# Performance work log

Hardware: AMD Instinct MI355X
Metric: run time of the kernel (lower is better)

The kernel has to match this reference:

```python
import jax, jax.numpy as jnp
import numpy as np

GRID_SIZE = 5
SPLINE_ORDER = 3
GRID_RANGE = (-1.0, 1.0)


def b_splines(x, grid, spline_order=SPLINE_ORDER):
    # x: [B, in], grid: [G] with G = grid_size + 2*spline_order + 1
    x = x[..., None]                      # [B, in, 1]
    g = grid[None, None, :]               # [1, 1, G]
    bases = ((x >= g[..., :-1]) & (x < g[..., 1:])).astype(x.dtype)  # [B, in, G-1]
    for k in range(1, spline_order + 1):
        left = (x - g[..., :-(k + 1)]) / (g[..., k:-1] - g[..., :-(k + 1)]) * bases[..., :-1]
        right = (g[..., k + 1:] - x) / (g[..., k + 1:] - g[..., 1:-k]) * bases[..., 1:]
        bases = left + right
    return bases                          # [B, in, grid_size + spline_order]


def setup_inputs() -> dict:
    key = jax.random.key(0)
    k1, k2, k3, k4 = jax.random.split(key, 4)
    B, IN, OUT = 32768, 256, 256
    n_coef = GRID_SIZE + SPLINE_ORDER  # 8
    h = (GRID_RANGE[1] - GRID_RANGE[0]) / GRID_SIZE
    grid = jnp.arange(-SPLINE_ORDER, GRID_SIZE + SPLINE_ORDER + 1, dtype=jnp.float32) * h + GRID_RANGE[0]  # [12]
    x = jax.random.normal(k1, (B, IN), dtype=jnp.float32)
    base_weight = jax.random.normal(k2, (OUT, IN), dtype=jnp.float32) * np.sqrt(2.0 / IN)
    spline_weight = jax.random.normal(k3, (OUT, IN, n_coef), dtype=jnp.float32) * (0.1 / GRID_SIZE)
    spline_scaler = jax.random.normal(k4, (OUT, IN), dtype=jnp.float32) * np.sqrt(2.0 / IN)
    return {"x": x, "base_weight": base_weight, "spline_weight": spline_weight,
            "spline_scaler": spline_scaler, "grid": grid}


def reference(x, base_weight, spline_weight, spline_scaler, grid):
    B = x.shape[0]
    out_features = base_weight.shape[0]
    # base branch: silu(x) @ base_weight^T
    base_out = jnp.matmul(jax.nn.silu(x), base_weight.T)  # [B, out]
    # spline branch
    bases = b_splines(x, grid)                             # [B, in, n_coef]
    scaled_w = spline_weight * spline_scaler[..., None]    # [out, in, n_coef]
    spline_out = jnp.matmul(bases.reshape(B, -1), scaled_w.reshape(out_features, -1).T)
    return base_out + spline_out
```

## Files before the change

### kernel.cpp

```cpp
#include <hip/hip_runtime.h>
#include <stdint.h>


#define IN_F 256
#define OUT_F 256
#define KDIM 2304
#define BK 64
#define NCHUNK (KDIM / BK)

typedef float f32x4 __attribute__((ext_vector_type(4)));
typedef short bf16x8 __attribute__((ext_vector_type(8)));

__device__ __forceinline__ uint32_t f2bf(float f) {
    union { float f; uint32_t u; } c; c.f = f;
    uint32_t u = c.u;
    return (u + 0x7FFFu + ((u >> 16) & 1u)) >> 16;
}

__device__ __forceinline__ uint32_t cvtpk(float lo, float hi) {
    uint32_t r;
    asm("v_cvt_pk_bf16_f32 %0, %1, %2" : "=v"(r) : "v"(lo), "v"(hi));
    return r;
}

__device__ __forceinline__ float silu_f(float v) {
    return v / (1.0f + __expf(-v));
}

__device__ __forceinline__ void block_sync_lds() {
    __builtin_amdgcn_sched_barrier(0);
    asm volatile("s_waitcnt lgkmcnt(0)" ::: "memory");
    __builtin_amdgcn_sched_barrier(0);
    __builtin_amdgcn_s_barrier();
    __builtin_amdgcn_sched_barrier(0);
}

__device__ __forceinline__ uint4 basis16(float xx) {
    float u = __builtin_fmaf(xx, 2.5f, 5.5f);
    float jf = floorf(u);
    float t = u - jf;
    int j0 = (int)jf;
    float t2 = t * t, t3 = t2 * t;
    float p3 = t3 * (1.0f / 6.0f);
    float p2 = __builtin_fmaf(t3, -0.5f,
               __builtin_fmaf(t2, 0.5f, __builtin_fmaf(t, 0.5f, 1.0f / 6.0f)));
    float p1 = __builtin_fmaf(t3, 0.5f, __builtin_fmaf(t2, -1.0f, 2.0f / 3.0f));
    float omt = 1.0f - t;
    float p0 = omt * omt * omt * (1.0f / 6.0f);
    const int s0 = j0 - 3;
    int ds = s0 >> 1;
    if ((unsigned)j0 > 10u) ds = 9;
    const bool odd = (s0 & 1) != 0;
    uint32_t v0 = cvtpk(odd ? 0.0f : p0, odd ? p0 : p1);
    uint32_t v1 = cvtpk(odd ? p1 : p2, odd ? p2 : p3);
    uint32_t v2 = odd ? cvtpk(p3, 0.0f) : 0u;
    uint4 r;
    r.x = (ds == 0) ? v0 : (ds == -1) ? v1 : (ds == -2) ? v2 : 0u;
    r.y = (ds == 1) ? v0 : (ds ==  0) ? v1 : (ds == -1) ? v2 : 0u;
    r.z = (ds == 2) ? v0 : (ds ==  1) ? v1 : (ds ==  0) ? v2 : 0u;
    r.w = (ds == 3) ? v0 : (ds ==  2) ? v1 : (ds ==  1) ? v2 : 0u;
    return r;
}

__device__ __forceinline__ size_t wcf_addr(int col, int k) {
    const int kc = k >> 6, kkh = (k >> 5) & 1, q = (k >> 3) & 3, e = k & 7;
    return ((size_t)((kc * 2 + kkh) * 16 + (col >> 4))) * 512 +
           (size_t)(q * 16 + (col & 15)) * 8 + e;
}

__global__ void build_w(const float* __restrict__ bw, const float* __restrict__ sw,
                        const float* __restrict__ ss, unsigned short* __restrict__ WcF) {
    const int o = blockIdx.x;
    const int i = threadIdx.x;
    WcF[wcf_addr(o, i)] = (unsigned short)f2bf(bw[o * IN_F + i]);
    const float scal = ss[o * IN_F + i];
    const float4* swv = reinterpret_cast<const float4*>(sw + (size_t)(o * IN_F + i) * 8);
    float4 s0 = swv[0], s1 = swv[1];
    uint4 wv;
    wv.x = f2bf(s0.x * scal) | (f2bf(s0.y * scal) << 16);
    wv.y = f2bf(s0.z * scal) | (f2bf(s0.w * scal) << 16);
    wv.z = f2bf(s1.x * scal) | (f2bf(s1.y * scal) << 16);
    wv.w = f2bf(s1.z * scal) | (f2bf(s1.w * scal) << 16);
    *reinterpret_cast<uint4*>(WcF + wcf_addr(o, IN_F + i * 8)) = wv;
}

__launch_bounds__(512, 2)
__global__ void kan_fused(const float* __restrict__ x, const unsigned short* __restrict__ WcF,
                          float* __restrict__ out) {
    __shared__ __align__(16) unsigned short As[4][128 * 64];

    const int bid = blockIdx.x;
    const int row0 = bid * 128;
    const int tid = threadIdx.x;
    const int lane = tid & 63;
    const int w = tid >> 6;
    const int wm = w >> 2;
    const int wn = w & 3;
    const int l15 = lane & 15;
    const int q = lane >> 4;

    const int erow = tid >> 2;
    const int qd   = tid & 3;

    f32x4 acc[4][4] = {};
    bf16x8 bE[8], bO[8];
    float2 x0, x1, x2, x3;

    const unsigned short* wbase = WcF + (size_t)lane * 8;

    auto load_b = [&](int kc, bf16x8* dst) {
#pragma unroll
        for (int nt = 0; nt < 4; ++nt)
#pragma unroll
            for (int kkh = 0; kkh < 2; ++kkh)
                dst[nt * 2 + kkh] = *reinterpret_cast<const bf16x8*>(
                    wbase + ((size_t)((kc * 2 + kkh) * 16 + wn * 4 + nt)) * 512);
    };
    auto load_x_silu = [&](int c, float4* xs4) {
        const float* xp = x + (size_t)(row0 + erow) * IN_F + c * 64 + qd * 16;
#pragma unroll
        for (int i = 0; i < 4; ++i)
            xs4[i] = reinterpret_cast<const float4*>(xp)[i];
    };
    auto load_x_bas = [&](int c, float2& v) {
        v = *reinterpret_cast<const float2*>(
            x + (size_t)(row0 + erow) * IN_F + (c - 4) * 8 + qd * 2);
    };
    auto expand_silu = [&](const float4* xs4, uint4& w0, uint4& w1) {
        w0.x = cvtpk(silu_f(xs4[0].x), silu_f(xs4[0].y));
        w0.y = cvtpk(silu_f(xs4[0].z), silu_f(xs4[0].w));
        w0.z = cvtpk(silu_f(xs4[1].x), silu_f(xs4[1].y));
        w0.w = cvtpk(silu_f(xs4[1].z), silu_f(xs4[1].w));
        w1.x = cvtpk(silu_f(xs4[2].x), silu_f(xs4[2].y));
        w1.y = cvtpk(silu_f(xs4[2].z), silu_f(xs4[2].w));
        w1.z = cvtpk(silu_f(xs4[3].x), silu_f(xs4[3].y));
        w1.w = cvtpk(silu_f(xs4[3].z), silu_f(xs4[3].w));
    };
    auto expand_bas = [&](float2 v, uint4& w0, uint4& w1) {
        w0 = basis16(v.x);
        w1 = basis16(v.y);
    };
    auto write_a = [&](unsigned short* Ab, const uint4& w0, const uint4& w1) {
        const int g0 = qd * 2;
        *reinterpret_cast<uint4*>(Ab + erow * 64 + ((g0 ^ (erow & 7)) << 3)) = w0;
        *reinterpret_cast<uint4*>(Ab + erow * 64 + (((g0 + 1) ^ (erow & 7)) << 3)) = w1;
    };
    auto mfma_chunk = [&](const unsigned short* Ab, const bf16x8* bv) {
#pragma unroll
        for (int kkh = 0; kkh < 2; ++kkh) {
            const int g0 = kkh * 4 + q;
#pragma unroll
            for (int mt = 0; mt < 4; ++mt) {
                int r = wm * 64 + mt * 16 + l15;
                bf16x8 a = *reinterpret_cast<const bf16x8*>(
                    Ab + r * 64 + ((g0 ^ (r & 7)) << 3));
                __builtin_amdgcn_s_setprio(1);
#pragma unroll
                for (int nt = 0; nt < 4; ++nt)
                    acc[mt][nt] = __builtin_amdgcn_mfma_f32_16x16x32_bf16(
                        a, bv[nt * 2 + kkh], acc[mt][nt], 0, 0, 0);
                __builtin_amdgcn_s_setprio(0);
            }
        }
    };

    float4 xf2[4], xf3[4];
    {
        float4 t4[4]; uint4 a, b;
        load_x_silu(0, t4); expand_silu(t4, a, b); write_a(&As[0][0], a, b);
        load_x_silu(1, t4); expand_silu(t4, a, b); write_a(&As[1][0], a, b);
    }
    load_x_silu(2, xf2);
    load_x_silu(3, xf3);
    load_x_bas(4, x0);
    load_x_bas(5, x1);
    load_b(0, bE);
    block_sync_lds();

    load_b(1, bO);
    load_x_bas(6, x2);
    load_x_bas(7, x3);
    {
        uint4 a2, b2, a3, b3;
        expand_silu(xf2, a2, b2); expand_silu(xf3, a3, b3);
        write_a(&As[2][0], a2, b2); write_a(&As[3][0], a3, b3);
    }
    mfma_chunk(&As[0][0], bE);
    load_b(2, bE);
    mfma_chunk(&As[1][0], bO);
    block_sync_lds();

    for (int t = 0; t < 8; ++t) {
        {
            const int kc = 4 * t + 2;
            load_b(kc + 1, bO);
            load_x_bas(kc + 4, x2);
            load_x_bas(kc + 5, x3);
            uint4 wa0, wb0, wa1, wb1;
            if (w < 4) {
                expand_bas(x0, wa0, wb0); expand_bas(x1, wa1, wb1);
                write_a(&As[0][0], wa0, wb0); write_a(&As[1][0], wa1, wb1);
                mfma_chunk(&As[2][0], bE);
                load_b(kc + 2, bE);
                mfma_chunk(&As[3][0], bO);
            } else {
                mfma_chunk(&As[2][0], bE);
                load_b(kc + 2, bE);
                mfma_chunk(&As[3][0], bO);
                expand_bas(x0, wa0, wb0); expand_bas(x1, wa1, wb1);
                write_a(&As[0][0], wa0, wb0); write_a(&As[1][0], wa1, wb1);
            }
            block_sync_lds();
        }
        {
            const int kc2 = 4 * t + 4;
            load_b(kc2 + 1, bO);
            if (kc2 + 5 < NCHUNK) {
                load_x_bas(kc2 + 4, x0);
                load_x_bas(kc2 + 5, x1);
            }
            uint4 wa0, wb0, wa1, wb1;
            if (w < 4) {
                expand_bas(x2, wa0, wb0); expand_bas(x3, wa1, wb1);
                write_a(&As[2][0], wa0, wb0); write_a(&As[3][0], wa1, wb1);
                mfma_chunk(&As[0][0], bE);
                load_b(kc2 + 2, bE);
                mfma_chunk(&As[1][0], bO);
            } else {
                mfma_chunk(&As[0][0], bE);
                load_b(kc2 + 2, bE);
                mfma_chunk(&As[1][0], bO);
                expand_bas(x2, wa0, wb0); expand_bas(x3, wa1, wb1);
                write_a(&As[2][0], wa0, wb0); write_a(&As[3][0], wa1, wb1);
            }
            block_sync_lds();
        }
    }

    load_b(35, bO);
    mfma_chunk(&As[2][0], bE);
    mfma_chunk(&As[3][0], bO);

#pragma unroll
    for (int mt = 0; mt < 4; ++mt) {
        int row = row0 + wm * 64 + mt * 16 + q * 4;
#pragma unroll
        for (int nt = 0; nt < 4; ++nt) {
            int col = wn * 64 + nt * 16 + l15;
#pragma unroll
            for (int r = 0; r < 4; ++r)
                out[(size_t)(row + r) * OUT_F + col] = acc[mt][nt][r];
        }
    }
}

extern "C" void kernel_launch(void* const* d_in, const int* in_sizes, int n_in,
                              void* d_out, int out_size, void* d_ws, size_t ws_size,
                              hipStream_t stream) {
    const float* x  = (const float*)d_in[0];
    const float* bw = (const float*)d_in[1];
    const float* sw = (const float*)d_in[2];
    const float* ss = (const float*)d_in[3];
    unsigned short* WcF = (unsigned short*)d_ws;

    build_w<<<dim3(OUT_F), dim3(IN_F), 0, stream>>>(bw, sw, ss, WcF);

    const int B_ROWS = in_sizes[0] / IN_F;
    kan_fused<<<dim3(B_ROWS / 128), dim3(512), 0, stream>>>(
        x, WcF, (float*)d_out);
}
```

Before: 137.1 us.

## Split K across wave groups with 64-row tiles and LDS reduction

Each block now covers 64 rows instead of 128. The two groups of four waves each handle one half of every 64-wide K chunk, and their partial accumulators are summed through LDS at the end. LDS use is halved and occupancy is targeted at 4 blocks per CU, aiming for more latency hiding and more blocks in flight. The cost is twice the B-weight traffic per output row, plus extra barriers and LDS round-trips for the reduction.

```diff
diff --git a/kernel.cpp b/kernel.cpp
--- a/kernel.cpp
+++ b/kernel.cpp
@@ -84,106 +84,91 @@
     *reinterpret_cast<uint4*>(WcF + wcf_addr(o, IN_F + i * 8)) = wv;
 }
 
-__launch_bounds__(512, 2)
+__launch_bounds__(512, 4)
 __global__ void kan_fused(const float* __restrict__ x, const unsigned short* __restrict__ WcF,
                           float* __restrict__ out) {
-    __shared__ __align__(16) unsigned short As[4][128 * 64];
+    __shared__ __align__(16) unsigned short As[4][64 * 64];
 
     const int bid = blockIdx.x;
-    const int row0 = bid * 128;
+    const int row0 = bid * 64;
     const int tid = threadIdx.x;
     const int lane = tid & 63;
     const int w = tid >> 6;
-    const int wm = w >> 2;
+    const int kh = w >> 2;
     const int wn = w & 3;
     const int l15 = lane & 15;
     const int q = lane >> 4;
 
-    const int erow = tid >> 2;
-    const int qd   = tid & 3;
+    const int erow = tid >> 3;
+    const int g8   = tid & 7;
 
     f32x4 acc[4][4] = {};
-    bf16x8 bE[8], bO[8];
-    float2 x0, x1, x2, x3;
+    bf16x8 bE[4], bO[4];
+    float x0, x1, x2, x3;
 
     const unsigned short* wbase = WcF + (size_t)lane * 8;
 
     auto load_b = [&](int kc, bf16x8* dst) {
 #pragma unroll
         for (int nt = 0; nt < 4; ++nt)
-#pragma unroll
-            for (int kkh = 0; kkh < 2; ++kkh)
-                dst[nt * 2 + kkh] = *reinterpret_cast<const bf16x8*>(
-                    wbase + ((size_t)((kc * 2 + kkh) * 16 + wn * 4 + nt)) * 512);
-    };
-    auto load_x_silu = [&](int c, float4* xs4) {
-        const float* xp = x + (size_t)(row0 + erow) * IN_F + c * 64 + qd * 16;
-#pragma unroll
-        for (int i = 0; i < 4; ++i)
-            xs4[i] = reinterpret_cast<const float4*>(xp)[i];
-    };
-    auto load_x_bas = [&](int c, float2& v) {
-        v = *reinterpret_cast<const float2*>(
-            x + (size_t)(row0 + erow) * IN_F + (c - 4) * 8 + qd * 2);
-    };
-    auto expand_silu = [&](const float4* xs4, uint4& w0, uint4& w1) {
-        w0.x = cvtpk(silu_f(xs4[0].x), silu_f(xs4[0].y));
-        w0.y = cvtpk(silu_f(xs4[0].z), silu_f(xs4[0].w));
-        w0.z = cvtpk(silu_f(xs4[1].x), silu_f(xs4[1].y));
-        w0.w = cvtpk(silu_f(xs4[1].z), silu_f(xs4[1].w));
-        w1.x = cvtpk(silu_f(xs4[2].x), silu_f(xs4[2].y));
-        w1.y = cvtpk(silu_f(xs4[2].z), silu_f(xs4[2].w));
-        w1.z = cvtpk(silu_f(xs4[3].x), silu_f(xs4[3].y));
-        w1.w = cvtpk(silu_f(xs4[3].z), silu_f(xs4[3].w));
-    };
-    auto expand_bas = [&](float2 v, uint4& w0, uint4& w1) {
-        w0 = basis16(v.x);
-        w1 = basis16(v.y);
-    };
-    auto write_a = [&](unsigned short* Ab, const uint4& w0, const uint4& w1) {
-        const int g0 = qd * 2;
-        *reinterpret_cast<uint4*>(Ab + erow * 64 + ((g0 ^ (erow & 7)) << 3)) = w0;
-        *reinterpret_cast<uint4*>(Ab + erow * 64 + (((g0 + 1) ^ (erow & 7)) << 3)) = w1;
+            dst[nt] = *reinterpret_cast<const bf16x8*>(
+                wbase + ((size_t)((kc * 2 + kh) * 16 + wn * 4 + nt)) * 512);
+    };
+    auto load_x_silu = [&](int c, float4& a, float4& b) {
+        const float* xp = x + (size_t)(row0 + erow) * IN_F + c * 64 + g8 * 8;
+        a = reinterpret_cast<const float4*>(xp)[0];
+        b = reinterpret_cast<const float4*>(xp)[1];
+    };
+    auto load_x_bas = [&](int c, float& v) {
+        v = x[(size_t)(row0 + erow) * IN_F + (c - 4) * 8 + g8];
+    };
+    auto expand_silu = [&](float4 a, float4 b, uint4& w0) {
+        w0.x = cvtpk(silu_f(a.x), silu_f(a.y));
+        w0.y = cvtpk(silu_f(a.z), silu_f(a.w));
+        w0.z = cvtpk(silu_f(b.x), silu_f(b.y));
+        w0.w = cvtpk(silu_f(b.z), silu_f(b.w));
+    };
+    auto write_a = [&](unsigned short* Ab, const uint4& w0) {
+        *reinterpret_cast<uint4*>(Ab + erow * 64 + ((g8 ^ (erow & 7)) << 3)) = w0;
     };
     auto mfma_chunk = [&](const unsigned short* Ab, const bf16x8* bv) {
-#pragma unroll
-        for (int kkh = 0; kkh < 2; ++kkh) {
-            const int g0 = kkh * 4 + q;
-#pragma unroll
-            for (int mt = 0; mt < 4; ++mt) {
-                int r = wm * 64 + mt * 16 + l15;
-                bf16x8 a = *reinterpret_cast<const bf16x8*>(
-                    Ab + r * 64 + ((g0 ^ (r & 7)) << 3));
-                __builtin_amdgcn_s_setprio(1);
-#pragma unroll
-                for (int nt = 0; nt < 4; ++nt)
-                    acc[mt][nt] = __builtin_amdgcn_mfma_f32_16x16x32_bf16(
-                        a, bv[nt * 2 + kkh], acc[mt][nt], 0, 0, 0);
-                __builtin_amdgcn_s_setprio(0);
-            }
-        }
-    };
-
-    float4 xf2[4], xf3[4];
+        const int g0 = kh * 4 + q;
+#pragma unroll
+        for (int mt = 0; mt < 4; ++mt) {
+            int r = mt * 16 + l15;
+            bf16x8 a = *reinterpret_cast<const bf16x8*>(
+                Ab + r * 64 + ((g0 ^ (r & 7)) << 3));
+            __builtin_amdgcn_s_setprio(1);
+#pragma unroll
+            for (int nt = 0; nt < 4; ++nt)
+                acc[mt][nt] = __builtin_amdgcn_mfma_f32_16x16x32_bf16(
+                    a, bv[nt], acc[mt][nt], 0, 0, 0);
+            __builtin_amdgcn_s_setprio(0);
+        }
+    };
+
+    float4 s2a, s2b, s3a, s3b;
     {
-        float4 t4[4]; uint4 a, b;
-        load_x_silu(0, t4); expand_silu(t4, a, b); write_a(&As[0][0], a, b);
-        load_x_silu(1, t4); expand_silu(t4, a, b); write_a(&As[1][0], a, b);
-    }
-    load_x_silu(2, xf2);
-    load_x_silu(3, xf3);
-    load_x_bas(4, x0);
-    load_x_bas(5, x1);
-    load_b(0, bE);
+        float4 a, b; uint4 t;
+        load_x_silu(0, a, b);
+        load_x_silu(1, s2a, s2b);
+        load_x_silu(2, s3a, s3b);
+        load_b(0, bE);
+        load_x_bas(4, x0);
+        load_x_bas(5, x1);
+        expand_silu(a, b, t);          write_a(&As[0][0], t);
+        expand_silu(s2a, s2b, t);      write_a(&As[1][0], t);
+        load_x_silu(3, s2a, s2b);
+    }
     block_sync_lds();
 
     load_b(1, bO);
-    load_x_bas(6, x2);
-    load_x_bas(7, x3);
     {
-        uint4 a2, b2, a3, b3;
-        expand_silu(xf2, a2, b2); expand_silu(xf3, a3, b3);
-        write_a(&As[2][0], a2, b2); write_a(&As[3][0], a3, b3);
+        uint4 a2, a3;
+        expand_silu(s3a, s3b, a2);
+        expand_silu(s2a, s2b, a3);
+        write_a(&As[2][0], a2);
+        write_a(&As[3][0], a3);
     }
     mfma_chunk(&As[0][0], bE);
     load_b(2, bE);
@@ -196,10 +181,10 @@
             load_b(kc + 1, bO);
             load_x_bas(kc + 4, x2);
             load_x_bas(kc + 5, x3);
-            uint4 wa0, wb0, wa1, wb1;
-            if (w < 4) {
-                expand_bas(x0, wa0, wb0); expand_bas(x1, wa1, wb1);
-                write_a(&As[0][0], wa0, wb0); write_a(&As[1][0], wa1, wb1);
+            uint4 wa0, wa1;
+            if (kh == 0) {
+                wa0 = basis16(x0); wa1 = basis16(x1);
+                write_a(&As[0][0], wa0); write_a(&As[1][0], wa1);
                 mfma_chunk(&As[2][0], bE);
                 load_b(kc + 2, bE);
                 mfma_chunk(&As[3][0], bO);
@@ -207,8 +192,8 @@
                 mfma_chunk(&As[2][0], bE);
                 load_b(kc + 2, bE);
                 mfma_chunk(&As[3][0], bO);
-                expand_bas(x0, wa0, wb0); expand_bas(x1, wa1, wb1);
-                write_a(&As[0][0], wa0, wb0); write_a(&As[1][0], wa1, wb1);
+                wa0 = basis16(x0); wa1 = basis16(x1);
+                write_a(&As[0][0], wa0); write_a(&As[1][0], wa1);
             }
             block_sync_lds();
         }
@@ -219,10 +204,10 @@
                 load_x_bas(kc2 + 4, x0);
                 load_x_bas(kc2 + 5, x1);
             }
-            uint4 wa0, wb0, wa1, wb1;
-            if (w < 4) {
-                expand_bas(x2, wa0, wb0); expand_bas(x3, wa1, wb1);
-                write_a(&As[2][0], wa0, wb0); write_a(&As[3][0], wa1, wb1);
+            uint4 wa0, wa1;
+            if (kh == 0) {
+                wa0 = basis16(x2); wa1 = basis16(x3);
+                write_a(&As[2][0], wa0); write_a(&As[3][0], wa1);
                 mfma_chunk(&As[0][0], bE);
                 load_b(kc2 + 2, bE);
                 mfma_chunk(&As[1][0], bO);
@@ -230,8 +215,8 @@
                 mfma_chunk(&As[0][0], bE);
                 load_b(kc2 + 2, bE);
                 mfma_chunk(&As[1][0], bO);
-                expand_bas(x2, wa0, wb0); expand_bas(x3, wa1, wb1);
-                write_a(&As[2][0], wa0, wb0); write_a(&As[3][0], wa1, wb1);
+                wa0 = basis16(x2); wa1 = basis16(x3);
+                write_a(&As[2][0], wa0); write_a(&As[3][0], wa1);
             }
             block_sync_lds();
         }
@@ -241,15 +226,34 @@
     mfma_chunk(&As[2][0], bE);
     mfma_chunk(&As[3][0], bO);
 
-#pragma unroll
-    for (int mt = 0; mt < 4; ++mt) {
-        int row = row0 + wm * 64 + mt * 16 + q * 4;
-#pragma unroll
-        for (int nt = 0; nt < 4; ++nt) {
-            int col = wn * 64 + nt * 16 + l15;
-#pragma unroll
-            for (int r = 0; r < 4; ++r)
-                out[(size_t)(row + r) * OUT_F + col] = acc[mt][nt][r];
+    float* red = reinterpret_cast<float*>(&As[0][0]);
+    const int slot = wn & 1;
+#pragma unroll
+    for (int round = 0; round < 2; ++round) {
+        block_sync_lds();
+        if ((wn >> 1) == round && kh == 1) {
+#pragma unroll
+            for (int mt = 0; mt < 4; ++mt)
+#pragma unroll
+                for (int nt = 0; nt < 4; ++nt)
+#pragma unroll
+                    for (int r = 0; r < 4; ++r)
+                        red[slot * 4096 + (mt * 16 + q * 4 + r) * 64 + nt * 16 + l15] =
+                            acc[mt][nt][r];
+        }
+        block_sync_lds();
+        if ((wn >> 1) == round && kh == 0) {
+#pragma unroll
+            for (int mt = 0; mt < 4; ++mt)
+#pragma unroll
+                for (int nt = 0; nt < 4; ++nt)
+#pragma unroll
+                    for (int r = 0; r < 4; ++r) {
+                        float v = acc[mt][nt][r] +
+                                  red[slot * 4096 + (mt * 16 + q * 4 + r) * 64 + nt * 16 + l15];
+                        out[(size_t)(row0 + mt * 16 + q * 4 + r) * OUT_F +
+                            wn * 64 + nt * 16 + l15] = v;
+                    }
         }
     }
 }
@@ -266,6 +270,6 @@
     build_w<<<dim3(OUT_F), dim3(IN_F), 0, stream>>>(bw, sw, ss, WcF);
 
     const int B_ROWS = in_sizes[0] / IN_F;
-    kan_fused<<<dim3(B_ROWS / 128), dim3(512), 0, stream>>>(
+    kan_fused<<<dim3(B_ROWS / 64), dim3(512), 0, stream>>>(
         x, WcF, (float*)d_out);
 }
```

After: 295.8 us. 2.16x slower.
